# Kernel optimization log

Hardware: AMD Instinct MI355X
Metric: run time of the kernel (lower is better)

## Reference

```python
import jax, jax.numpy as jnp
import numpy as np

BN_EPS = 1e-5
CLAMP = 1e-10


def _three_nn(q, p):
    # q: (B,N,3) query points, p: (B,M,3) reference points
    # returns dist (B,N,3) euclidean distance to 3 nearest, idx (B,N,3)
    d2 = (jnp.sum(q * q, -1)[:, :, None] + jnp.sum(p * p, -1)[:, None, :]
          - 2.0 * jnp.einsum('bnd,bmd->bnm', q, p))  # (B,N,M)
    neg_vals, idx = jax.lax.top_k(-d2, 3)
    dist = jnp.sqrt(jnp.maximum(-neg_vals, 1e-20))
    return dist, idx


def _gather(feats_t, idx):
    # feats_t: (B,M,C), idx: (B,N,3) -> (B,N,3,C)
    return jax.vmap(lambda f, i: f[i])(feats_t, idx)


def _conv_bn_relu(x, W, b, g, beta):
    # x: (B,Cin,N); 1x1 Conv1d + BatchNorm1d (training-mode batch stats) + relu
    y = jnp.einsum('oc,bcn->bon', W, x) + b[None, :, None]
    mean = jnp.mean(y, axis=(0, 2), keepdims=True)
    var = jnp.mean((y - mean) ** 2, axis=(0, 2), keepdims=True)
    y = (y - mean) * jax.lax.rsqrt(var + BN_EPS)
    y = y * g[None, :, None] + beta[None, :, None]
    return jax.nn.relu(y)


def setup_inputs() -> dict:
    key = jax.random.key(0)
    ks = jax.random.split(key, 10)
    B, N, M, C2, C1 = 4, 8192, 2048, 256, 128
    inp = {
        'xyz1': jax.random.normal(ks[0], (B, 3, N), jnp.float32),
        'xyz2': jax.random.normal(ks[1], (B, 3, M), jnp.float32),
        'norm1': jax.random.normal(ks[2], (B, 3, N), jnp.float32),
        'norm2': jax.random.normal(ks[3], (B, 3, M), jnp.float32),
        'points1': jax.random.normal(ks[4], (B, C1, N), jnp.float32),
        'points2': jax.random.normal(ks[5], (B, C2, M), jnp.float32),
        'W0': jax.random.normal(ks[6], (256, C2 + C1), jnp.float32) * 0.05,
        'b0': jax.random.normal(ks[7], (256,), jnp.float32) * 0.05,
        'g0': jnp.ones((256,), jnp.float32),
        'be0': jnp.zeros((256,), jnp.float32),
        'W1': jax.random.normal(ks[8], (128, 256), jnp.float32) * 0.05,
        'b1': jax.random.normal(ks[9], (128,), jnp.float32) * 0.05,
        'g1': jnp.ones((128,), jnp.float32),
        'be1': jnp.zeros((128,), jnp.float32),
    }
    return inp


def reference(xyz1, xyz2, norm1, norm2, points1, points2,
              W0, b0, g0, be0, W1, b1, g1, be1):
    B, _, N = xyz1.shape
    # 3-NN search
    dist, idx = _three_nn(jnp.transpose(xyz1, (0, 2, 1)),
                          jnp.transpose(xyz2, (0, 2, 1)))  # (B,N,3)
    # normal distance between query normals and gathered neighbor normals
    grouped_norm = _gather(jnp.transpose(norm2, (0, 2, 1)), idx)        # (B,N,3,3)
    diff = jnp.transpose(norm1, (0, 2, 1))[:, :, None, :] - grouped_norm
    norm_dist = jnp.sqrt(jnp.sum(diff * diff, -1))                       # (B,N,3)
    # distance weights
    recip_dist = 1.0 / jnp.maximum(dist, CLAMP)
    weight = recip_dist / jnp.sum(recip_dist, 2, keepdims=True)
    # normal weights
    recip_nd = 1.0 / jnp.maximum(norm_dist, CLAMP)
    norm_weight = recip_nd / jnp.sum(recip_nd, 2, keepdims=True)
    weight = weight * norm_weight                                        # (B,N,3)
    # three_interpolate: weighted gather of points2
    gathered_pts = _gather(jnp.transpose(points2, (0, 2, 1)), idx)       # (B,N,3,C)
    interpolated = jnp.einsum('bnkc,bnk->bcn', gathered_pts, weight)     # (B,C,N)
    new_points = jnp.concatenate([interpolated, points1], axis=1)        # (B,C+C1,N)
    new_points = _conv_bn_relu(new_points, W0, b0, g0, be0)
    new_points = _conv_bn_relu(new_points, W1, b1, g1, be1)
    return new_points
```

## Files before the change

### kernel.cpp

```cpp
#include <hip/hip_runtime.h>
#include <hip/hip_bf16.h>
#include <cstdint>
#include <cstddef>

static constexpr int BB   = 4;
static constexpr int NN   = 8192;
static constexpr int MM   = 2048;
static constexpr int C1   = 128;
static constexpr int C2   = 256;
static constexpr int CH0  = C2 + C1;
static constexpr int O0   = 256;
static constexpr int O1   = 128;
static constexpr int NCOL = BB * NN;
static constexpr float BN_EPS = 1e-5f;

using u16 = unsigned short;
typedef __attribute__((ext_vector_type(8))) short short8;
typedef __attribute__((ext_vector_type(4))) float f32x4;

static __device__ __forceinline__ float bf2f(u16 u) {
    union { unsigned int i; float f; } v; v.i = ((unsigned int)u) << 16; return v.f;
}
static __device__ __forceinline__ u16 f2bf(float f) {
    union { float f; unsigned int i; } v; v.f = f;
    unsigned int r = (v.i + 0x7fffu + ((v.i >> 16) & 1u)) >> 16;
    return (u16)r;
}

__global__ __launch_bounds__(256) void prep_kernel(const float* __restrict__ points2,
                                                   u16* __restrict__ p2T,
                                                   const float* __restrict__ points1,
                                                   u16* __restrict__ p1T,
                                                   const float* __restrict__ W0f,
                                                   u16* __restrict__ W0b,
                                                   const float* __restrict__ W1f,
                                                   u16* __restrict__ W1b) {
    __shared__ float tile[32][33];
    int id = blockIdx.x;
    int t  = threadIdx.x;
    if (id < 6144) {
        const float* in; u16* out; int R, C, b, c0, r0;
        if (id < 2048) {
            in = points2; out = p2T; R = C2; C = MM;
            b = id >> 9; int rem = id & 511;
            c0 = (rem & 63) * 32; r0 = (rem >> 6) * 32;
        } else {
            int id2 = id - 2048;
            in = points1; out = p1T; R = C1; C = NN;
            b = id2 >> 10; int rem = id2 & 1023;
            c0 = (rem & 255) * 32; r0 = (rem >> 8) * 32;
        }
        int tx = t & 31, ty = t >> 5;
        const float* pin = in + (size_t)b * R * C;
        u16* pout = out + (size_t)b * R * C;
#pragma unroll
        for (int j = 0; j < 4; ++j) {
            int r = ty + j * 8;
            tile[r][tx] = pin[(size_t)(r0 + r) * C + (c0 + tx)];
        }
        __syncthreads();
#pragma unroll
        for (int j = 0; j < 4; ++j) {
            int c = ty + j * 8;
            pout[(size_t)(c0 + c) * R + (r0 + tx)] = f2bf(tile[tx][c]);
        }
    } else {
        int i = (id - 6144) * 256 + t;
        if (i < O0 * CH0) W0b[i] = f2bf(W0f[i]);
        else {
            int i2 = i - O0 * CH0;
            if (i2 < O1 * O0) W1b[i2] = f2bf(W1f[i2]);
        }
    }
}

__global__ __launch_bounds__(256) void three_nn_kernel(const float* __restrict__ xyz1,
                                                       const float* __restrict__ xyz2,
                                                       const float* __restrict__ norm1,
                                                       const float* __restrict__ norm2,
                                                       int* __restrict__ idxOut,
                                                       float* __restrict__ wOut) {
#pragma clang fp contract(off)
    constexpr int CH = 1024;
    __shared__ float4 pts[CH];
    int b    = blockIdx.x >> 8;
    int nblk = blockIdx.x & 255;
    int t    = threadIdx.x;
    int j    = t & 7;

    int n = nblk * 32 + (t >> 3);
    const float* x1 = xyz1 + (size_t)b * 3 * NN;
    float qx = x1[n], qy = x1[NN + n], qz = x1[2 * NN + n];
    float qq = (qx * qx + qy * qy) + qz * qz;

    const float* x2 = xyz2 + (size_t)b * 3 * MM;

    float d0 = 3.4e38f, d1 = 3.4e38f, d2v = 3.4e38f;
    int   i0 = 0, i1 = 0, i2 = 0;

    for (int chunk = 0; chunk < MM / CH; ++chunk) {
        __syncthreads();
        for (int i = t; i < CH; i += 256) {
            int m = chunk * CH + i;
            float px = x2[m];
            float py = x2[MM + m];
            float pz = x2[2 * MM + m];
            float pp = (px * px + py * py) + pz * pz;
            pts[i] = make_float4(px, py, pz, pp);
        }
        __syncthreads();

#pragma unroll 8
        for (int s = 0; s < CH / 8; ++s) {
            int ml = s * 8 + j;
            float4 P = pts[ml];
            float qp = (qx * P.x + qy * P.y) + qz * P.z;
            float d  = (qq + P.w) - 2.0f * qp;
            if (d < d2v) {
                int m = chunk * CH + ml;
                if (d < d1) {
                    if (d < d0) { d2v = d1; i2 = i1; d1 = d0; i1 = i0; d0 = d; i0 = m; }
                    else        { d2v = d1; i2 = i1; d1 = d;  i1 = m; }
                } else          { d2v = d;  i2 = m; }
            }
        }
    }

#pragma unroll
    for (int k = 1; k <= 4; k <<= 1) {
        float e0 = __shfl_xor(d0, k, 64), e1 = __shfl_xor(d1, k, 64), e2 = __shfl_xor(d2v, k, 64);
        int   f0 = __shfl_xor(i0, k, 64), f1 = __shfl_xor(i1, k, 64), f2 = __shfl_xor(i2, k, 64);
        float ed[3] = {e0, e1, e2}; int ef[3] = {f0, f1, f2};
#pragma unroll
        for (int e = 0; e < 3; ++e) {
            float dd = ed[e]; int ff = ef[e];
            bool b2 = (dd < d2v) || (dd == d2v && ff < i2);
            if (b2) {
                bool b1 = (dd < d1) || (dd == d1 && ff < i1);
                if (b1) {
                    d2v = d1; i2 = i1;
                    bool b0 = (dd < d0) || (dd == d0 && ff < i0);
                    if (b0) { d1 = d0; i1 = i0; d0 = dd; i0 = ff; }
                    else    { d1 = dd; i1 = ff; }
                } else { d2v = dd; i2 = ff; }
            }
        }
    }

    if (j == 0) {
        float s0 = sqrtf(fmaxf(d0, 1e-20f));
        float s1 = sqrtf(fmaxf(d1, 1e-20f));
        float s2 = sqrtf(fmaxf(d2v, 1e-20f));
        float r0 = 1.0f / fmaxf(s0, 1e-10f);
        float r1 = 1.0f / fmaxf(s1, 1e-10f);
        float r2 = 1.0f / fmaxf(s2, 1e-10f);
        float rs = (r0 + r1) + r2;
        float w0 = r0 / rs, w1 = r1 / rs, w2 = r2 / rs;

        const float* nm1 = norm1 + (size_t)b * 3 * NN;
        const float* nm2 = norm2 + (size_t)b * 3 * MM;
        float ax = nm1[n], ay = nm1[NN + n], az = nm1[2 * NN + n];
        float nd[3]; int ii[3] = {i0, i1, i2};
#pragma unroll
        for (int k = 0; k < 3; ++k) {
            int ik = ii[k];
            float dx = ax - nm2[ik];
            float dy = ay - nm2[MM + ik];
            float dz = az - nm2[2 * MM + ik];
            nd[k] = sqrtf((dx * dx + dy * dy) + dz * dz);
        }
        float m0 = 1.0f / fmaxf(nd[0], 1e-10f);
        float m1 = 1.0f / fmaxf(nd[1], 1e-10f);
        float m2 = 1.0f / fmaxf(nd[2], 1e-10f);
        float ms = (m0 + m1) + m2;

        int col = b * NN + n;
        idxOut[col * 3 + 0] = i0;
        idxOut[col * 3 + 1] = i1;
        idxOut[col * 3 + 2] = i2;
        wOut[col * 3 + 0] = w0 * (m0 / ms);
        wOut[col * 3 + 1] = w1 * (m1 / ms);
        wOut[col * 3 + 2] = w2 * (m2 / ms);
    }
}

template <int KDIM, int LDC, int COLT, int MODE>
__global__ __launch_bounds__(256) void gemm_bt_kernel(const u16* __restrict__ A,
                                                      const u16* __restrict__ Bt,
                                                      const u16* __restrict__ p1T,
                                                      const int* __restrict__ idx,
                                                      const float* __restrict__ w,
                                                      u16* __restrict__ Ct,
                                                      const float* __restrict__ bias,
                                                      const float* __restrict__ redB,
                                                      const float* __restrict__ gB,
                                                      const float* __restrict__ beB,
                                                      float invN,
                                                      float* __restrict__ partials) {
    constexpr int KT  = KDIM / 64;
    constexpr int NI  = COLT / 32;
    constexpr int ASZ = 128 * 64;
    constexpr int BSZ = COLT * 64;
    __shared__ u16 smem[2 * ASZ + 2 * BSZ];
    __shared__ float sSc[MODE == 1 ? KDIM : 1];
    __shared__ float sSh[MODE == 1 ? KDIM : 1];

    int t   = threadIdx.x;
    int l   = t & 63;
    int wv  = t >> 6;
    int rl  = l >> 3;
    int cg  = ((l & 7) ^ rl) * 8;
    int mb0 = blockIdx.y * 128;
    int cb0 = blockIdx.x * COLT;
    int lm  = l & 15;
    int q   = l >> 4;
    int wm0 = (wv & 1) * 64;
    int wn0 = (wv >> 1) * (COLT / 2);

    const u16* Abase = A + (size_t)mb0 * KDIM;

    int vi0 = 0, vi1 = 0, vi2 = 0;
    float vw0 = 0.f, vw1 = 0.f, vw2 = 0.f;
    const u16* p2base = nullptr;
    if (MODE == 2) {
        int colg = cb0 + (t >> 2);
        vi0 = idx[colg * 3 + 0]; vi1 = idx[colg * 3 + 1]; vi2 = idx[colg * 3 + 2];
        vw0 = w[colg * 3 + 0];   vw1 = w[colg * 3 + 1];   vw2 = w[colg * 3 + 2];
        p2base = Bt + (size_t)(cb0 >> 13) * MM * C2;
    }
    if (MODE == 1) {
        int by = t >> 7, chL = t & 127;
        const float* base = redB + (size_t)by * 8 * 256;
        float s = 0.f, s2 = 0.f;
#pragma unroll
        for (int i = 0; i < 8; ++i) {
            s  += base[i * 256 + chL];
            s2 += base[i * 256 + 128 + chL];
        }
        float mean = s * invN;
        float var  = fmaxf(s2 * invN - mean * mean, 0.f);
        float inv  = rsqrtf(var + BN_EPS);
        float sc   = gB[t] * inv;
        sSc[t] = sc;
        sSh[t] = beB[t] - mean * sc;
        __syncthreads();
    }

    auto stage = [&](int buf, int k0) {
#pragma unroll
        for (int iss = 0; iss < 4; ++iss) {
            int row = wv * 32 + iss * 8;
            const u16* g = Abase + (size_t)(row + rl) * KDIM + k0 + cg;
            __builtin_amdgcn_global_load_lds(
                (const __attribute__((address_space(1))) unsigned int*)g,
                (__attribute__((address_space(3))) unsigned int*)(&smem[buf * ASZ + row * 64]),
                16, 0, 0);
        }
        if (MODE == 0) {
#pragma unroll
            for (int iss = 0; iss < COLT / 32; ++iss) {
                int row = wv * (COLT / 4) + iss * 8;
                const u16* g = Bt + (size_t)(cb0 + row + rl) * KDIM + k0 + cg;
                __builtin_amdgcn_global_load_lds(
                    (const __attribute__((address_space(1))) unsigned int*)g,
                    (__attribute__((address_space(3))) unsigned int*)(&smem[2 * ASZ + buf * BSZ + row * 64]),
                    16, 0, 0);
            }
        } else if (MODE == 1) {
            int row = t >> 2;
            int kc  = (t & 3) * 16;
            const u16* gp = Bt + (size_t)(cb0 + row) * KDIM + k0 + kc;
            union { uint4 v; u16 u[8]; } lo, hi;
            lo.v = *(const uint4*)gp;
            hi.v = *(const uint4*)(gp + 8);
#pragma unroll
            for (int e = 0; e < 8; ++e) {
                float f0 = bf2f(lo.u[e]);
                lo.u[e] = f2bf(fmaxf(f0 * sSc[k0 + kc + e] + sSh[k0 + kc + e], 0.f));
                float f1 = bf2f(hi.u[e]);
                hi.u[e] = f2bf(fmaxf(f1 * sSc[k0 + kc + 8 + e] + sSh[k0 + kc + 8 + e], 0.f));
            }
            int c0 = kc >> 3;
            u16* dstB = &smem[2 * ASZ + buf * BSZ + row * 64];
            *(uint4*)&dstB[((c0)     ^ (row & 7)) * 8] = lo.v;
            *(uint4*)&dstB[((c0 + 1) ^ (row & 7)) * 8] = hi.v;
        } else {
            if (k0 < C2) {
                int row = t >> 2;
                int kc  = (t & 3) * 16;
                const u16* bp = p2base + k0 + kc;
                const u16* r0p = bp + (size_t)vi0 * C2;
                const u16* r1p = bp + (size_t)vi1 * C2;
                const u16* r2p = bp + (size_t)vi2 * C2;
                union { uint4 v; u16 u[8]; } x0, x1, x2, y0, y1, y2, lo, hi;
                x0.v = *(const uint4*)r0p; y0.v = *(const uint4*)(r0p + 8);
                x1.v = *(const uint4*)r1p; y1.v = *(const uint4*)(r1p + 8);
                x2.v = *(const uint4*)r2p; y2.v = *(const uint4*)(r2p + 8);
#pragma unroll
                for (int e = 0; e < 8; ++e) {
                    lo.u[e] = f2bf(vw0 * bf2f(x0.u[e]) + vw1 * bf2f(x1.u[e]) + vw2 * bf2f(x2.u[e]));
                    hi.u[e] = f2bf(vw0 * bf2f(y0.u[e]) + vw1 * bf2f(y1.u[e]) + vw2 * bf2f(y2.u[e]));
                }
                int c0 = kc >> 3;
                u16* dstB = &smem[2 * ASZ + buf * BSZ + row * 64];
                *(uint4*)&dstB[((c0)     ^ (row & 7)) * 8] = lo.v;
                *(uint4*)&dstB[((c0 + 1) ^ (row & 7)) * 8] = hi.v;
            } else {
#pragma unroll
                for (int iss = 0; iss < COLT / 32; ++iss) {
                    int row = wv * (COLT / 4) + iss * 8;
                    const u16* g = p1T + (size_t)(cb0 + row + rl) * C1 + (k0 - C2) + cg;
                    __builtin_amdgcn_global_load_lds(
                        (const __attribute__((address_space(1))) unsigned int*)g,
                        (__attribute__((address_space(3))) unsigned int*)(&smem[2 * ASZ + buf * BSZ + row * 64]),
                        16, 0, 0);
                }
            }
        }
    };

    f32x4 acc[4][NI] = {};

    stage(0, 0);
    for (int kt = 0; kt < KT; ++kt) {
        __syncthreads();
        if (kt + 1 < KT) stage((kt + 1) & 1, (kt + 1) * 64);
        const u16* As = &smem[(kt & 1) * ASZ];
        const u16* Bs = &smem[2 * ASZ + (kt & 1) * BSZ];
#pragma unroll
        for (int ks = 0; ks < 2; ++ks) {
            int csw = ((ks * 4 + q) ^ (lm & 7)) * 8;
            short8 av[4], bv[NI];
#pragma unroll
            for (int mi = 0; mi < 4; ++mi)
                av[mi] = *(const short8*)&As[(wm0 + mi * 16 + lm) * 64 + csw];
#pragma unroll
            for (int ni = 0; ni < NI; ++ni)
                bv[ni] = *(const short8*)&Bs[(wn0 + ni * 16 + lm) * 64 + csw];
#pragma unroll
            for (int mi = 0; mi < 4; ++mi)
#pragma unroll
                for (int ni = 0; ni < NI; ++ni)
                    acc[mi][ni] = __builtin_amdgcn_mfma_f32_16x16x32_bf16(
                        av[mi], bv[ni], acc[mi][ni], 0, 0, 0);
        }
    }

    u16*   Cs   = smem;
    float* reds = (float*)&smem[COLT * 136];

    __syncthreads();
    if (t < 256) reds[t] = 0.f;
    __syncthreads();

#pragma unroll
    for (int mi = 0; mi < 4; ++mi) {
        int chL = wm0 + mi * 16 + q * 4;
        float bv4[4];
#pragma unroll
        for (int r = 0; r < 4; ++r) bv4[r] = bias[mb0 + chL + r];
        float s[4]  = {0.f, 0.f, 0.f, 0.f};
        float s2[4] = {0.f, 0.f, 0.f, 0.f};
#pragma unroll
        for (int ni = 0; ni < NI; ++ni) {
            int colL = wn0 + ni * 16 + lm;
            union { u16 u[4]; uint2 d; } pk;
#pragma unroll
            for (int r = 0; r < 4; ++r) {
                float v = acc[mi][ni][r] + bv4[r];
                s[r]  += v;
                s2[r] += v * v;
                pk.u[r] = f2bf(v);
            }
            *(uint2*)&Cs[colL * 136 + chL] = pk.d;
        }
#pragma unroll
        for (int r = 0; r < 4; ++r) {
            float a = s[r], b2 = s2[r];
#pragma unroll
            for (int off = 1; off < 16; off <<= 1) {
                a  += __shfl_xor(a, off, 64);
                b2 += __shfl_xor(b2, off, 64);
            }
            if (lm == 0) {
                atomicAdd(&reds[chL + r], a);
                atomicAdd(&reds[128 + chL + r], b2);
            }
        }
    }
    __syncthreads();

    for (int u = t; u < COLT * 2; u += 256) {
        int c = u >> 1, h = u & 1;
        const u16* src = &Cs[c * 136 + h * 64];
        u16* dst = Ct + (size_t)(cb0 + c) * LDC + mb0 + h * 64;
#pragma unroll
        for (int jj = 0; jj < 8; ++jj)
            *(uint4*)(dst + jj * 8) = *(const uint4*)(src + jj * 8);
    }
    partials[((size_t)blockIdx.y * gridDim.x + blockIdx.x) * 256 + t] = reds[t];
}

__global__ __launch_bounds__(256) void reduce_partials_kernel(const float* __restrict__ in,
                                                              float* __restrict__ out,
                                                              int chunk) {
    int t = threadIdx.x, r = blockIdx.x;
    const float* base = in + (size_t)r * chunk * 256;
    float s = 0.f;
#pragma unroll 8
    for (int i = 0; i < chunk; ++i) s += base[(size_t)i * 256 + t];
    out[(size_t)r * 256 + t] = s;
}

__global__ __launch_bounds__(256) void finalize_kernel(const u16* __restrict__ y1T,
                                                       const float* __restrict__ red1,
                                                       const float* __restrict__ g1,
                                                       const float* __restrict__ be1,
                                                       float invN,
                                                       float* __restrict__ out) {
    __shared__ float tile[64][129];
    __shared__ float sc[O1], sh[O1];
    int t  = threadIdx.x;
    int b  = blockIdx.y;
    int n0 = blockIdx.x * 64;

    if (t < O1) {
        float s = 0.f, s2 = 0.f;
#pragma unroll
        for (int i = 0; i < 16; ++i) {
            s  += red1[i * 256 + t];
            s2 += red1[i * 256 + 128 + t];
        }
        float mean = s * invN;
        float var  = fmaxf(s2 * invN - mean * mean, 0.f);
        float inv  = rsqrtf(var + BN_EPS);
        float scv  = g1[t] * inv;
        sc[t] = scv;
        sh[t] = be1[t] - mean * scv;
    }
    __syncthreads();

#pragma unroll
    for (int it = 0; it < 32; ++it) {
        int flat = it * 256 + t;
        int cl = flat >> 7;
        int c  = flat & 127;
        int col = b * NN + n0 + cl;
        float v = bf2f(y1T[(size_t)col * O1 + c]);
        tile[cl][c] = fmaxf(v * sc[c] + sh[c], 0.f);
    }
    __syncthreads();
#pragma unroll
    for (int it = 0; it < 32; ++it) {
        int flat = it * 256 + t;
        int c  = flat >> 6;
        int nl = flat & 63;
        out[(size_t)b * O1 * NN + (size_t)c * NN + n0 + nl] = tile[nl][c];
    }
}

extern "C" void kernel_launch(void* const* d_in, const int* in_sizes, int n_in,
                              void* d_out, int out_size, void* d_ws, size_t ws_size,
                              hipStream_t stream) {
    (void)in_sizes; (void)n_in; (void)out_size; (void)ws_size;

    const float* xyz1    = (const float*)d_in[0];
    const float* xyz2    = (const float*)d_in[1];
    const float* norm1   = (const float*)d_in[2];
    const float* norm2   = (const float*)d_in[3];
    const float* points1 = (const float*)d_in[4];
    const float* points2 = (const float*)d_in[5];
    const float* W0f     = (const float*)d_in[6];
    const float* b0      = (const float*)d_in[7];
    const float* g0      = (const float*)d_in[8];
    const float* be0     = (const float*)d_in[9];
    const float* W1f     = (const float*)d_in[10];
    const float* b1      = (const float*)d_in[11];
    const float* g1      = (const float*)d_in[12];
    const float* be1     = (const float*)d_in[13];
    float* out = (float*)d_out;

    char* w8 = (char*)d_ws;
    size_t off = 0;
    auto carve = [&](size_t bytes) { void* p = w8 + off; off += (bytes + 255) & ~(size_t)255; return p; };
    int*   idxW   = (int*)  carve((size_t)NCOL * 3 * sizeof(int));
    float* wW     = (float*)carve((size_t)NCOL * 3 * sizeof(float));
    u16*   p2T    = (u16*)  carve((size_t)BB * MM * C2 * 2);
    u16*   p1T    = (u16*)  carve((size_t)BB * NN * C1 * 2);
    u16*   W0b    = (u16*)  carve((size_t)O0 * CH0 * 2);
    u16*   W1b    = (u16*)  carve((size_t)O1 * O0 * 2);
    u16*   y0T    = (u16*)  carve((size_t)NCOL * O0 * 2);
    u16*   y1T    = (u16*)  carve((size_t)NCOL * O1 * 2);
    float* part0  = (float*)carve((size_t)1024 * 256 * sizeof(float));
    float* part1  = (float*)carve((size_t)512 * 256 * sizeof(float));
    float* red0   = (float*)carve((size_t)16 * 256 * sizeof(float));
    float* red1   = (float*)carve((size_t)16 * 256 * sizeof(float));

    const float invN = 1.0f / (float)NCOL;

    prep_kernel<<<6656, 256, 0, stream>>>(points2, p2T, points1, p1T,
                                          W0f, W0b, W1f, W1b);

    three_nn_kernel<<<BB * (NN / 32), 256, 0, stream>>>(xyz1, xyz2, norm1, norm2, idxW, wW);

    gemm_bt_kernel<CH0, O0, 64, 2><<<dim3(NCOL / 64, O0 / 128), 256, 0, stream>>>(
        W0b, p2T, p1T, idxW, wW, y0T, b0, nullptr, nullptr, nullptr, invN, part0);
    reduce_partials_kernel<<<16, 256, 0, stream>>>(part0, red0, 64);

    gemm_bt_kernel<O0, O1, 64, 1><<<dim3(NCOL / 64, O1 / 128), 256, 0, stream>>>(
        W1b, y0T, nullptr, nullptr, nullptr, y1T, b1, red0, g0, be0, invN, part1);
    reduce_partials_kernel<<<16, 256, 0, stream>>>(part1, red1, 32);

    finalize_kernel<<<dim3(NN / 64, BB), 256, 0, stream>>>(y1T, red1, g1, be1, invN, out);
}
```

Before: 199.4 us.

## Fuse prep and 3-NN kernels, replace partial reductions with atomic accumulation

Merges the transpose/cast prep kernel and the three_nn kernel into one launch that dispatches work by block index, and also zeroes the BN-statistics buffers in it. The GEMM kernels now atomically add their per-block channel sums into a small set of striped records instead of writing full partials, which removes both reduce_partials launches. The next consumer sums across those records. This cuts three kernel launches and the intermediate partial traffic, at the cost of atomic contention and a larger, mixed-workload first kernel. The unused MODE 0 B-staging path is also deleted.

Result: faster. 189.9 us (-4.8%).

```diff
diff --git a/kernel.cpp b/kernel.cpp
--- a/kernel.cpp
+++ b/kernel.cpp
@@ -14,6 +14,9 @@
 static constexpr int NCOL = BB * NN;
 static constexpr float BN_EPS = 1e-5f;
 
+static constexpr int REC0 = 64;
+static constexpr int REC1 = 32;
+
 using u16 = unsigned short;
 typedef __attribute__((ext_vector_type(8))) short short8;
 typedef __attribute__((ext_vector_type(4))) float f32x4;
@@ -27,65 +30,67 @@
     return (u16)r;
 }
 
-__global__ __launch_bounds__(256) void prep_kernel(const float* __restrict__ points2,
-                                                   u16* __restrict__ p2T,
-                                                   const float* __restrict__ points1,
-                                                   u16* __restrict__ p1T,
-                                                   const float* __restrict__ W0f,
-                                                   u16* __restrict__ W0b,
-                                                   const float* __restrict__ W1f,
-                                                   u16* __restrict__ W1b) {
-    __shared__ float tile[32][33];
+__global__ __launch_bounds__(256) void fused_pre_kernel(
+        const float* __restrict__ xyz1,  const float* __restrict__ xyz2,
+        const float* __restrict__ norm1, const float* __restrict__ norm2,
+        int* __restrict__ idxOut, float* __restrict__ wOut,
+        const float* __restrict__ points2, u16* __restrict__ p2T,
+        const float* __restrict__ points1, u16* __restrict__ p1T,
+        const float* __restrict__ W0f, u16* __restrict__ W0b,
+        const float* __restrict__ W1f, u16* __restrict__ W1b,
+        float* __restrict__ part0, float* __restrict__ part1) {
+#pragma clang fp contract(off)
+    __shared__ union { float4 pts[1024]; float tile[32][33]; } sm;
     int id = blockIdx.x;
     int t  = threadIdx.x;
-    if (id < 6144) {
-        const float* in; u16* out; int R, C, b, c0, r0;
-        if (id < 2048) {
-            in = points2; out = p2T; R = C2; C = MM;
-            b = id >> 9; int rem = id & 511;
-            c0 = (rem & 63) * 32; r0 = (rem >> 6) * 32;
+
+    if (id >= 7680) {
+        int flat = (id - 7680) * 256 + t;
+        if (flat < 2 * REC0 * 256) part0[flat] = 0.f;
+        else part1[flat - 2 * REC0 * 256] = 0.f;
+        return;
+    }
+    if (id >= 1024) {
+        int pid = id - 1024;
+        if (pid < 6144) {
+            const float* in; u16* out; int R, C, b, c0, r0;
+            if (pid < 2048) {
+                in = points2; out = p2T; R = C2; C = MM;
+                b = pid >> 9; int rem = pid & 511;
+                c0 = (rem & 63) * 32; r0 = (rem >> 6) * 32;
+            } else {
+                int id2 = pid - 2048;
+                in = points1; out = p1T; R = C1; C = NN;
+                b = id2 >> 10; int rem = id2 & 1023;
+                c0 = (rem & 255) * 32; r0 = (rem >> 8) * 32;
+            }
+            int tx = t & 31, ty = t >> 5;
+            const float* pin = in + (size_t)b * R * C;
+            u16* pout = out + (size_t)b * R * C;
+#pragma unroll
+            for (int j = 0; j < 4; ++j) {
+                int r = ty + j * 8;
+                sm.tile[r][tx] = pin[(size_t)(r0 + r) * C + (c0 + tx)];
+            }
+            __syncthreads();
+#pragma unroll
+            for (int j = 0; j < 4; ++j) {
+                int c = ty + j * 8;
+                pout[(size_t)(c0 + c) * R + (r0 + tx)] = f2bf(sm.tile[tx][c]);
+            }
         } else {
-            int id2 = id - 2048;
-            in = points1; out = p1T; R = C1; C = NN;
-            b = id2 >> 10; int rem = id2 & 1023;
-            c0 = (rem & 255) * 32; r0 = (rem >> 8) * 32;
-        }
-        int tx = t & 31, ty = t >> 5;
-        const float* pin = in + (size_t)b * R * C;
-        u16* pout = out + (size_t)b * R * C;
-#pragma unroll
-        for (int j = 0; j < 4; ++j) {
-            int r = ty + j * 8;
-            tile[r][tx] = pin[(size_t)(r0 + r) * C + (c0 + tx)];
-        }
-        __syncthreads();
-#pragma unroll
-        for (int j = 0; j < 4; ++j) {
-            int c = ty + j * 8;
-            pout[(size_t)(c0 + c) * R + (r0 + tx)] = f2bf(tile[tx][c]);
-        }
-    } else {
-        int i = (id - 6144) * 256 + t;
-        if (i < O0 * CH0) W0b[i] = f2bf(W0f[i]);
-        else {
-            int i2 = i - O0 * CH0;
-            if (i2 < O1 * O0) W1b[i2] = f2bf(W1f[i2]);
-        }
-    }
-}
-
-__global__ __launch_bounds__(256) void three_nn_kernel(const float* __restrict__ xyz1,
-                                                       const float* __restrict__ xyz2,
-                                                       const float* __restrict__ norm1,
-                                                       const float* __restrict__ norm2,
-                                                       int* __restrict__ idxOut,
-                                                       float* __restrict__ wOut) {
-#pragma clang fp contract(off)
-    constexpr int CH = 1024;
-    __shared__ float4 pts[CH];
-    int b    = blockIdx.x >> 8;
-    int nblk = blockIdx.x & 255;
-    int t    = threadIdx.x;
+            int i = (pid - 6144) * 256 + t;
+            if (i < O0 * CH0) W0b[i] = f2bf(W0f[i]);
+            else {
+                int i2 = i - O0 * CH0;
+                if (i2 < O1 * O0) W1b[i2] = f2bf(W1f[i2]);
+            }
+        }
+        return;
+    }
+
+    int b    = id >> 8;
+    int nblk = id & 255;
     int j    = t & 7;
 
     int n = nblk * 32 + (t >> 3);
@@ -98,26 +103,26 @@
     float d0 = 3.4e38f, d1 = 3.4e38f, d2v = 3.4e38f;
     int   i0 = 0, i1 = 0, i2 = 0;
 
-    for (int chunk = 0; chunk < MM / CH; ++chunk) {
+    for (int chunk = 0; chunk < MM / 1024; ++chunk) {
         __syncthreads();
-        for (int i = t; i < CH; i += 256) {
-            int m = chunk * CH + i;
+        for (int i = t; i < 1024; i += 256) {
+            int m = chunk * 1024 + i;
             float px = x2[m];
             float py = x2[MM + m];
             float pz = x2[2 * MM + m];
             float pp = (px * px + py * py) + pz * pz;
-            pts[i] = make_float4(px, py, pz, pp);
+            sm.pts[i] = make_float4(px, py, pz, pp);
         }
         __syncthreads();
 
 #pragma unroll 8
-        for (int s = 0; s < CH / 8; ++s) {
+        for (int s = 0; s < 1024 / 8; ++s) {
             int ml = s * 8 + j;
-            float4 P = pts[ml];
+            float4 P = sm.pts[ml];
             float qp = (qx * P.x + qy * P.y) + qz * P.z;
             float d  = (qq + P.w) - 2.0f * qp;
             if (d < d2v) {
-                int m = chunk * CH + ml;
+                int m = chunk * 1024 + ml;
                 if (d < d1) {
                     if (d < d0) { d2v = d1; i2 = i1; d1 = d0; i1 = i0; d0 = d; i0 = m; }
                     else        { d2v = d1; i2 = i1; d1 = d;  i1 = m; }
@@ -230,10 +235,10 @@
     }
     if (MODE == 1) {
         int by = t >> 7, chL = t & 127;
-        const float* base = redB + (size_t)by * 8 * 256;
+        const float* base = redB + (size_t)by * REC0 * 256;
         float s = 0.f, s2 = 0.f;
-#pragma unroll
-        for (int i = 0; i < 8; ++i) {
+#pragma unroll 8
+        for (int i = 0; i < REC0; ++i) {
             s  += base[i * 256 + chL];
             s2 += base[i * 256 + 128 + chL];
         }
@@ -256,17 +261,7 @@
                 (__attribute__((address_space(3))) unsigned int*)(&smem[buf * ASZ + row * 64]),
                 16, 0, 0);
         }
-        if (MODE == 0) {
-#pragma unroll
-            for (int iss = 0; iss < COLT / 32; ++iss) {
-                int row = wv * (COLT / 4) + iss * 8;
-                const u16* g = Bt + (size_t)(cb0 + row + rl) * KDIM + k0 + cg;
-                __builtin_amdgcn_global_load_lds(
-                    (const __attribute__((address_space(1))) unsigned int*)g,
-                    (__attribute__((address_space(3))) unsigned int*)(&smem[2 * ASZ + buf * BSZ + row * 64]),
-                    16, 0, 0);
-            }
-        } else if (MODE == 1) {
+        if (MODE == 1) {
             int row = t >> 2;
             int kc  = (t & 3) * 16;
             const u16* gp = Bt + (size_t)(cb0 + row) * KDIM + k0 + kc;
@@ -398,22 +393,13 @@
         for (int jj = 0; jj < 8; ++jj)
             *(uint4*)(dst + jj * 8) = *(const uint4*)(src + jj * 8);
     }
-    partials[((size_t)blockIdx.y * gridDim.x + blockIdx.x) * 256 + t] = reds[t];
-}
-
-__global__ __launch_bounds__(256) void reduce_partials_kernel(const float* __restrict__ in,
-                                                              float* __restrict__ out,
-                                                              int chunk) {
-    int t = threadIdx.x, r = blockIdx.x;
-    const float* base = in + (size_t)r * chunk * 256;
-    float s = 0.f;
-#pragma unroll 8
-    for (int i = 0; i < chunk; ++i) s += base[(size_t)i * 256 + t];
-    out[(size_t)r * 256 + t] = s;
+    int recIdx = (MODE == 2) ? (blockIdx.y * REC0 + (blockIdx.x & (REC0 - 1)))
+                             : (blockIdx.x & (REC1 - 1));
+    atomicAdd(&partials[(size_t)recIdx * 256 + t], reds[t]);
 }
 
 __global__ __launch_bounds__(256) void finalize_kernel(const u16* __restrict__ y1T,
-                                                       const float* __restrict__ red1,
+                                                       const float* __restrict__ part1,
                                                        const float* __restrict__ g1,
                                                        const float* __restrict__ be1,
                                                        float invN,
@@ -426,10 +412,10 @@
 
     if (t < O1) {
         float s = 0.f, s2 = 0.f;
-#pragma unroll
-        for (int i = 0; i < 16; ++i) {
-            s  += red1[i * 256 + t];
-            s2 += red1[i * 256 + 128 + t];
+#pragma unroll 8
+        for (int i = 0; i < REC1; ++i) {
+            s  += part1[i * 256 + t];
+            s2 += part1[i * 256 + 128 + t];
         }
         float mean = s * invN;
         float var  = fmaxf(s2 * invN - mean * mean, 0.f);
@@ -491,25 +477,20 @@
     u16*   W1b    = (u16*)  carve((size_t)O1 * O0 * 2);
     u16*   y0T    = (u16*)  carve((size_t)NCOL * O0 * 2);
     u16*   y1T    = (u16*)  carve((size_t)NCOL * O1 * 2);
-    float* part0  = (float*)carve((size_t)1024 * 256 * sizeof(float));
-    float* part1  = (float*)carve((size_t)512 * 256 * sizeof(float));
-    float* red0   = (float*)carve((size_t)16 * 256 * sizeof(float));
-    float* red1   = (float*)carve((size_t)16 * 256 * sizeof(float));
+    float* part0  = (float*)carve((size_t)2 * REC0 * 256 * sizeof(float));
+    float* part1  = (float*)carve((size_t)REC1 * 256 * sizeof(float));
 
     const float invN = 1.0f / (float)NCOL;
 
-    prep_kernel<<<6656, 256, 0, stream>>>(points2, p2T, points1, p1T,
-                                          W0f, W0b, W1f, W1b);
-
-    three_nn_kernel<<<BB * (NN / 32), 256, 0, stream>>>(xyz1, xyz2, norm1, norm2, idxW, wW);
+    fused_pre_kernel<<<7840, 256, 0, stream>>>(
+        xyz1, xyz2, norm1, norm2, idxW, wW,
+        points2, p2T, points1, p1T, W0f, W0b, W1f, W1b, part0, part1);
 
     gemm_bt_kernel<CH0, O0, 64, 2><<<dim3(NCOL / 64, O0 / 128), 256, 0, stream>>>(
         W0b, p2T, p1T, idxW, wW, y0T, b0, nullptr, nullptr, nullptr, invN, part0);
-    reduce_partials_kernel<<<16, 256, 0, stream>>>(part0, red0, 64);
 
     gemm_bt_kernel<O0, O1, 64, 1><<<dim3(NCOL / 64, O1 / 128), 256, 0, stream>>>(
-        W1b, y0T, nullptr, nullptr, nullptr, y1T, b1, red0, g0, be0, invN, part1);
-    reduce_partials_kernel<<<16, 256, 0, stream>>>(part1, red1, 32);
-
-    finalize_kernel<<<dim3(NN / 64, BB), 256, 0, stream>>>(y1T, red1, g1, be1, invN, out);
-}
+        W1b, y0T, nullptr, nullptr, nullptr, y1T, b1, part0, g0, be0, invN, part1);
+
+    finalize_kernel<<<dim3(NN / 64, BB), 256, 0, stream>>>(y1T, part1, g1, be1, invN, out);
+}
```
